# Optimization experiments

Hardware: AMD Instinct MI355X
Metric: run time of the kernel (lower is better)

Reference implementation:

```python
import jax, jax.numpy as jnp
import numpy as np
import math

BATCH, TBINS, SPATIAL = 16, 8, 16
WIN, SHIFT = 8, 4
DIM, HEADS = 1024, 16
HD = DIM // HEADS
N = WIN * WIN          # tokens per window = 64
NW = (SPATIAL // WIN) ** 2  # windows per image = 4
HIDDEN = 4 * DIM


def _static_buffers():
    ws = WIN
    # continuous relative coords table (signed log-spaced), [(2ws-1)^2, 2]
    c = np.arange(-(ws - 1), ws, dtype=np.float32) / (ws - 1)
    c = np.sign(c) * np.log2(1.0 + np.abs(c))
    gh, gw = np.meshgrid(c, c, indexing='ij')
    table = np.stack([gh, gw], axis=-1).reshape(-1, 2).astype(np.float32)
    # relative position index, [N, N]
    coords = np.stack(np.meshgrid(np.arange(ws), np.arange(ws), indexing='ij')).reshape(2, -1)
    rel = (coords[:, :, None] - coords[:, None, :]).transpose(1, 2, 0)
    rel[..., 0] += ws - 1
    rel[..., 1] += ws - 1
    rel[..., 0] *= 2 * ws - 1
    rp_idx = rel.sum(-1)  # [N, N] int
    # shifted-window attention mask, [NW, N, N]
    img = np.zeros((SPATIAL, SPATIAL), dtype=np.float32)
    slices = [slice(0, -ws), slice(-ws, -SHIFT), slice(-SHIFT, None)]
    cnt = 0
    for hs in slices:
        for wsl in slices:
            img[hs, wsl] = cnt
            cnt += 1
    mw = img.reshape(SPATIAL // ws, ws, SPATIAL // ws, ws).transpose(0, 2, 1, 3).reshape(-1, ws * ws)
    diff = mw[:, None, :] - mw[:, :, None]  # matches unsqueeze(1) - unsqueeze(2)
    attn_mask = np.where(diff != 0, np.float32(-100.0), np.float32(0.0))
    return jnp.asarray(table), jnp.asarray(rp_idx), jnp.asarray(attn_mask)

CPB_TABLE, RP_IDX, ATTN_MASK = _static_buffers()


def _window_partition(x):  # [B, H, W, C] -> [B*nW, ws, ws, C]
    b, h, w, c = x.shape
    x = x.reshape(b, h // WIN, WIN, w // WIN, WIN, c).transpose(0, 1, 3, 2, 4, 5)
    return x.reshape(-1, WIN, WIN, c)


def _window_reverse(win, h, w):  # [B*nW, ws, ws, C] -> [B, H, W, C]
    b = win.shape[0] // ((h // WIN) * (w // WIN))
    x = win.reshape(b, h // WIN, w // WIN, WIN, WIN, -1).transpose(0, 1, 3, 2, 4, 5)
    return x.reshape(b, h, w, -1)


def _layernorm(x, g, b):
    m = jnp.mean(x, -1, keepdims=True)
    v = jnp.mean((x - m) ** 2, -1, keepdims=True)
    return (x - m) * jax.lax.rsqrt(v + 1e-5) * g + b


def _l2norm(x):
    return x / jnp.maximum(jnp.linalg.norm(x, axis=-1, keepdims=True), 1e-12)


def setup_inputs() -> dict:
    key = jax.random.key(0)
    ks = jax.random.split(key, 16)
    s = 0.02
    inp = {
        'x': jax.random.normal(ks[0], (BATCH, TBINS * SPATIAL * SPATIAL, DIM), jnp.float32),
        'qkv_w': jax.random.normal(ks[1], (3 * DIM, DIM), jnp.float32) * s,
        'q_bias': jnp.zeros((DIM,), jnp.float32),
        'v_bias': jnp.zeros((DIM,), jnp.float32),
        'logit_scale': jnp.full((HEADS, 1, 1), math.log(10.0), jnp.float32),
        'cpb_w1': jax.random.normal(ks[2], (512, 2), jnp.float32) * s,
        'cpb_b1': jnp.zeros((512,), jnp.float32),
        'cpb_w2': jax.random.normal(ks[3], (HEADS, 512), jnp.float32) * s,
        'proj_w': jax.random.normal(ks[4], (DIM, DIM), jnp.float32) * s,
        'proj_b': jnp.zeros((DIM,), jnp.float32),
        'norm1_w': jnp.ones((DIM,), jnp.float32),
        'norm1_b': jnp.zeros((DIM,), jnp.float32),
        'fc1_w': jax.random.normal(ks[5], (HIDDEN, DIM), jnp.float32) * s,
        'fc1_b': jnp.zeros((HIDDEN,), jnp.float32),
        'fc2_w': jax.random.normal(ks[6], (DIM, HIDDEN), jnp.float32) * s,
        'fc2_b': jnp.zeros((DIM,), jnp.float32),
        'norm2_w': jnp.ones((DIM,), jnp.float32),
        'norm2_b': jnp.zeros((DIM,), jnp.float32),
    }
    return inp


def reference(x, qkv_w, q_bias, v_bias, logit_scale, cpb_w1, cpb_b1, cpb_w2,
              proj_w, proj_b, norm1_w, norm1_b, fc1_w, fc1_b, fc2_w, fc2_b,
              norm2_w, norm2_b):
    B, L, C = x.shape
    xs = x.reshape(B * TBINS, SPATIAL, SPATIAL, C)
    shortcut = xs
    # cyclic shift
    shifted = jnp.roll(xs, shift=(-SHIFT, -SHIFT), axis=(1, 2))
    xw = _window_partition(shifted).reshape(-1, N, C)  # [Bw, N, C]
    Bw = xw.shape[0]

    # qkv with q/v bias only (no k bias)
    qkv_bias = jnp.concatenate([q_bias, jnp.zeros_like(v_bias), v_bias])
    qkv = xw @ qkv_w.T + qkv_bias
    qkv = qkv.reshape(Bw, N, 3, HEADS, HD).transpose(2, 0, 3, 1, 4)
    q, k, v = qkv[0], qkv[1], qkv[2]  # [Bw, h, N, hd]

    # cosine attention with clamped learnable logit scale
    attn = jnp.einsum('bhnd,bhmd->bhnm', _l2norm(q), _l2norm(k))
    scale = jnp.exp(jnp.minimum(logit_scale, math.log(100.0)))  # [h,1,1]
    attn = attn * scale[None]

    # continuous relative position bias via CPB-MLP
    tbl = jax.nn.relu(CPB_TABLE @ cpb_w1.T + cpb_b1) @ cpb_w2.T  # [(2ws-1)^2, h]
    tbl = 16.0 * jax.nn.sigmoid(tbl)
    bias = tbl[RP_IDX.reshape(-1)].reshape(N, N, HEADS).transpose(2, 0, 1)  # [h,N,N]
    attn = attn + bias[None]

    # shift mask
    attn = attn.reshape(Bw // NW, NW, HEADS, N, N) + ATTN_MASK[None, :, None]
    attn = attn.reshape(Bw, HEADS, N, N)
    attn = jax.nn.softmax(attn, axis=-1)

    out = jnp.einsum('bhnm,bhmd->bhnd', attn, v)
    out = out.transpose(0, 2, 1, 3).reshape(Bw, N, C)
    out = out @ proj_w.T + proj_b

    out = _window_reverse(out.reshape(-1, WIN, WIN, C), SPATIAL, SPATIAL)
    out = jnp.roll(out, shift=(SHIFT, SHIFT), axis=(1, 2))

    # SwinV2 post-norm residuals
    xs = shortcut + _layernorm(out, norm1_w, norm1_b)
    h = jax.nn.gelu(xs @ fc1_w.T + fc1_b, approximate=False) @ fc2_w.T + fc2_b
    xs = xs + _layernorm(h, norm2_w, norm2_b)
    return xs.reshape(B, L, C)
```

## Files before the change

### kernel.cpp

```cpp
#include <hip/hip_runtime.h>
#include <hip/hip_bf16.h>
#include <math.h>

typedef __hip_bfloat16 bf16;
typedef __attribute__((ext_vector_type(8))) short short8;
typedef __attribute__((ext_vector_type(4))) short short4v;
typedef __attribute__((ext_vector_type(4))) float floatx4;
typedef __attribute__((ext_vector_type(2))) unsigned int uint2v;

#define DEV static __device__ __forceinline__

DEV float bf2f(unsigned short u) {
  union { unsigned int i; float f; } x;
  x.i = ((unsigned int)u) << 16;
  return x.f;
}
DEV unsigned short f2bf_bits(float f) {
  union { bf16 h; unsigned short u; } x;
  x.h = __float2bfloat16(f);
  return x.u;
}
DEV short8 cvt8(float4 a, float4 b) {
  short8 r;
  r[0] = (short)f2bf_bits(a.x); r[1] = (short)f2bf_bits(a.y);
  r[2] = (short)f2bf_bits(a.z); r[3] = (short)f2bf_bits(a.w);
  r[4] = (short)f2bf_bits(b.x); r[5] = (short)f2bf_bits(b.y);
  r[6] = (short)f2bf_bits(b.z); r[7] = (short)f2bf_bits(b.w);
  return r;
}

DEV float gelu_fast(float v) {
  float y = v * (1.5957691216f + 0.0713548163f * v * v);
  return __fdividef(v, 1.f + __expf(-y));
}

DEV void gload_lds16(const unsigned short* g, unsigned short* l) {
  __builtin_amdgcn_global_load_lds((const __attribute__((address_space(1))) void*)g,
                                   (__attribute__((address_space(3))) void*)l,
                                   16, 0, 0);
}

DEV unsigned lds_addr(const void* p) {
  return (unsigned)(unsigned long long)(const __attribute__((address_space(3))) char*)p;
}

DEV int gather_win_row(int wr) {
  int bw = wr >> 6, n = wr & 63;
  int bt = bw >> 2, w2 = bw & 3;
  int wi = w2 >> 1, wj = w2 & 1;
  int r = n >> 3, c = n & 7;
  int sr = (wi * 8 + r + 4) & 15;
  int sc = (wj * 8 + c + 4) & 15;
  return bt * 256 + sr * 16 + sc;
}

enum { BIAS_SIMPLE = 0, BIAS_QKV = 1 };
enum { ACT_NONE = 0, ACT_GELU = 1 };

__global__ __launch_bounds__(256) void cvt_bf16(const float* __restrict__ in,
                                                bf16* __restrict__ out, int n) {
  int i = (blockIdx.x * 256 + threadIdx.x) * 8;
  if (i >= n) return;
  float4 a = *reinterpret_cast<const float4*>(in + i);
  float4 b = *reinterpret_cast<const float4*>(in + i + 4);
  *reinterpret_cast<short8*>((unsigned short*)out + i) = cvt8(a, b);
}

#define VMCNT(N_) asm volatile("s_waitcnt vmcnt(" #N_ ")" ::: "memory")
#define WAITLGKM() do { asm volatile("s_waitcnt lgkmcnt(0)" ::: "memory"); \
                        __builtin_amdgcn_sched_barrier(0); } while (0)
#define BARRIER() __builtin_amdgcn_s_barrier()
#define DSR(dst, addr, OFF) \
  asm volatile("ds_read_b128 %0, %1 offset:" #OFF : "=v"(dst) : "v"(addr) : "memory")

#define STG8(BUF, ISB, KS, KT) do { \
    unsigned short* d_ = (unsigned short*)(smem + (BUF) * 65536 + (ISB) * 32768 + (KS) * 16384); \
    gload_lds16(((ISB) ? bgp[0] : agp[0]) + (KT) * 64 + (KS) * 32, d_ + tid * 8); \
    gload_lds16(((ISB) ? bgp[1] : agp[1]) + (KT) * 64 + (KS) * 32, d_ + 4096 + tid * 8); \
  } while (0)

#define RD_A8(CUR, KS, IH) do { \
    unsigned a_ = smemBase + (CUR) * 65536 + (KS) * 16384 + aB0 + (IH) * 4096; \
    DSR(af[0], a_, 0); DSR(af[1], a_, 1024); DSR(af[2], a_, 2048); DSR(af[3], a_, 3072); \
  } while (0)

#define RD_B8(CUR, KS) do { \
    unsigned b_ = smemBase + (CUR) * 65536 + 32768 + (KS) * 16384 + bB0; \
    DSR(bfr[0], b_, 0); DSR(bfr[1], b_, 1024); DSR(bfr[2], b_, 2048); DSR(bfr[3], b_, 3072); \
  } while (0)

#define MFMA16(IH) do { \
    __builtin_amdgcn_s_setprio(1); \
    _Pragma("unroll") \
    for (int i_ = 0; i_ < 4; ++i_) \
      _Pragma("unroll") \
      for (int j_ = 0; j_ < 4; ++j_) \
        acc[(IH) * 4 + i_][j_] = __builtin_amdgcn_mfma_f32_16x16x32_bf16( \
            af[i_], bfr[j_], acc[(IH) * 4 + i_][j_], 0, 0, 0); \
    __builtin_amdgcn_s_setprio(0); \
  } while (0)

template <int GATHER, int BIASMODE, int ACT>
__global__ __launch_bounds__(512, 2) void gemm8p(
    const unsigned short* __restrict__ A, const unsigned short* __restrict__ B,
    const float* __restrict__ bias0, const float* __restrict__ bias1,
    bf16* __restrict__ C, int M, int N, int K)
{
  extern __shared__ __align__(16) char smem[];
  const int tid = threadIdx.x;
  const int lane = tid & 63;
  const int wave = tid >> 6;
  const int wm = wave >> 2, wn = wave & 3;
  const int l15 = lane & 15, g = lane >> 4;
  const int xr = (l15 >> 1) & 3;

  const int gy = gridDim.y;
  const int nwg = gridDim.x * gy;
  int lin = blockIdx.y * gridDim.x + blockIdx.x;
  if ((nwg & 7) == 0) lin = (lin & 7) * (nwg >> 3) + (lin >> 3);
  const int tileM = (lin / gy) * 256;
  const int tileN = (lin % gy) * 256;

  const unsigned short* agp[2];
  const unsigned short* bgp[2];
#pragma unroll
  for (int u = 0; u < 2; ++u) {
    int s = u * 512 + tid;
    int row = s >> 2;
    int dslot = (s & 3) ^ ((s >> 3) & 3);
    int gr = tileM + row;
    int sr = GATHER ? gather_win_row(gr) : gr;
    agp[u] = A + (size_t)sr * (size_t)K + dslot * 8;
    bgp[u] = B + (size_t)(tileN + row) * (size_t)K + dslot * 8;
  }

  const unsigned smemBase = lds_addr(smem);
  const unsigned aB0 = (unsigned)((wm * 128 + l15) * 64 + ((g ^ xr) * 16));
  const unsigned bB0 = (unsigned)((wn * 64 + l15) * 64 + ((g ^ xr) * 16));

  floatx4 acc[8][4];
#pragma unroll
  for (int i = 0; i < 8; ++i)
#pragma unroll
    for (int j = 0; j < 4; ++j) acc[i][j] = (floatx4){0.f, 0.f, 0.f, 0.f};

  short8 af[4], bfr[4];
  const int NT = K >> 6;
  int cur = 0;

  STG8(0, 0, 0, 0); STG8(0, 1, 0, 0); STG8(0, 0, 1, 0); STG8(0, 1, 1, 0);
  VMCNT(0);
  BARRIER();

  for (int t = 0; t < NT - 1; ++t) {
    const int nb = cur ^ 1;
    RD_B8(cur, 0); RD_A8(cur, 0, 0);
    STG8(nb, 0, 0, t + 1);
    BARRIER(); WAITLGKM(); MFMA16(0); BARRIER();
    RD_A8(cur, 0, 1);
    STG8(nb, 1, 0, t + 1);
    VMCNT(4);
    BARRIER(); WAITLGKM(); MFMA16(1); BARRIER();
    RD_B8(cur, 1); RD_A8(cur, 1, 0);
    STG8(nb, 0, 1, t + 1);
    BARRIER(); WAITLGKM(); MFMA16(0); BARRIER();
    RD_A8(cur, 1, 1);
    STG8(nb, 1, 1, t + 1);
    VMCNT(4);
    BARRIER(); WAITLGKM(); MFMA16(1); BARRIER();
    cur = nb;
  }
  RD_B8(cur, 0); RD_A8(cur, 0, 0);
  BARRIER(); WAITLGKM(); MFMA16(0); BARRIER();
  RD_A8(cur, 0, 1);
  VMCNT(0);
  BARRIER(); WAITLGKM(); MFMA16(1); BARRIER();
  RD_B8(cur, 1); RD_A8(cur, 1, 0);
  BARRIER(); WAITLGKM(); MFMA16(0); BARRIER();
  RD_A8(cur, 1, 1);
  WAITLGKM(); MFMA16(1);

  __syncthreads();
  unsigned short* sh16 = (unsigned short*)smem;
  const int q = l15;
  float bv[4];
#pragma unroll
  for (int j = 0; j < 4; ++j) {
    const int colG = tileN + wn * 64 + j * 16 + q;
    if (BIASMODE == BIAS_QKV) {
      bv[j] = (colG < 1024) ? bias0[colG] : (colG < 2048 ? 0.f : bias1[colG - 2048]);
    } else {
      bv[j] = bias0[colG];
    }
  }
#pragma unroll
  for (int h = 0; h < 2; ++h) {
    if (wm == h) {
#pragma unroll
      for (int i = 0; i < 8; ++i)
#pragma unroll
        for (int j = 0; j < 4; ++j)
#pragma unroll
          for (int r = 0; r < 4; ++r) {
            float v = acc[i][j][r] + bv[j];
            if (ACT == ACT_GELU) v = gelu_fast(v);
            sh16[(i * 16 + g * 4 + r) * 264 + wn * 64 + j * 16 + q] = f2bf_bits(v);
          }
    }
    __syncthreads();
#pragma unroll
    for (int pass = 0; pass < 8; ++pass) {
      const int idx = pass * 512 + tid;
      const int row = idx >> 5, c16 = idx & 31;
      uint4 val = *reinterpret_cast<const uint4*>(&sh16[row * 264 + c16 * 8]);
      *reinterpret_cast<uint4*>(
          (unsigned short*)C + (size_t)(tileM + h * 128 + row) * (size_t)N +
          tileN + c16 * 8) = val;
    }
    __syncthreads();
  }
}

template <int GATHER, int BIASMODE, int ACT>
__global__ __launch_bounds__(256, 2) void gemm_bt(
    const unsigned short* __restrict__ A, const unsigned short* __restrict__ B,
    const float* __restrict__ bias0, const float* __restrict__ bias1,
    bf16* __restrict__ C, int M, int N, int K)
{
  __shared__ __align__(16) unsigned short sh[128 * 136];
  unsigned short* As = sh;
  unsigned short* Bs = sh + 8192;

  const int tid = threadIdx.x;
  const int lane = tid & 63;
  const int wave = tid >> 6;
  const int waveM = wave >> 1, waveN = wave & 1;
  const int tileM = blockIdx.x * 128, tileN = blockIdx.y * 128;

  const int row0 = tid >> 3;
  const int kOff = (tid & 7) * 8;

  const unsigned short* ag[4];
  const unsigned short* bg[4];
  unsigned short* al[4];
  unsigned short* bl[4];
#pragma unroll
  for (int t = 0; t < 4; ++t) {
    int gr = tileM + row0 + 32 * t;
    int sr = GATHER ? gather_win_row(gr) : gr;
    ag[t] = A + (size_t)sr * (size_t)K + (size_t)kOff;
    bg[t] = B + (size_t)(tileN + row0 + 32 * t) * (size_t)K + (size_t)kOff;
    al[t] = &As[(row0 + 32 * t) * 64 + kOff];
    bl[t] = &Bs[(row0 + 32 * t) * 64 + kOff];
  }

  floatx4 acc[4][4];
#pragma unroll
  for (int i = 0; i < 4; ++i)
#pragma unroll
    for (int j = 0; j < 4; ++j) acc[i][j] = (floatx4){0.f, 0.f, 0.f, 0.f};

  for (int k0 = 0; k0 < K; k0 += 64) {
#pragma unroll
    for (int t = 0; t < 4; ++t) {
      gload_lds16(ag[t] + k0, al[t]);
      gload_lds16(bg[t] + k0, bl[t]);
    }
    __syncthreads();
#pragma unroll
    for (int ks = 0; ks < 2; ++ks) {
      const int kk = ks * 32 + (lane >> 4) * 8;
      short8 afv[4], bfv[4];
#pragma unroll
      for (int i = 0; i < 4; ++i)
        afv[i] = *reinterpret_cast<const short8*>(
            &As[(waveM * 64 + i * 16 + (lane & 15)) * 64 + kk]);
#pragma unroll
      for (int j = 0; j < 4; ++j)
        bfv[j] = *reinterpret_cast<const short8*>(
            &Bs[(waveN * 64 + j * 16 + (lane & 15)) * 64 + kk]);
#pragma unroll
      for (int i = 0; i < 4; ++i)
#pragma unroll
        for (int j = 0; j < 4; ++j)
          acc[i][j] = __builtin_amdgcn_mfma_f32_16x16x32_bf16(afv[i], bfv[j], acc[i][j], 0, 0, 0);
    }
    __syncthreads();
  }

#pragma unroll
  for (int j = 0; j < 4; ++j) {
    const int colL = waveN * 64 + j * 16 + (lane & 15);
    const int colG = tileN + colL;
    float bv;
    if (BIASMODE == BIAS_QKV) {
      if (colG < 1024) bv = bias0[colG];
      else if (colG < 2048) bv = 0.f;
      else bv = bias1[colG - 2048];
    } else {
      bv = bias0[colG];
    }
#pragma unroll
    for (int i = 0; i < 4; ++i) {
      const int rL = waveM * 64 + i * 16 + ((lane >> 4) * 4);
#pragma unroll
      for (int r = 0; r < 4; ++r) {
        float v = acc[i][j][r] + bv;
        if (ACT == ACT_GELU) v = gelu_fast(v);
        sh[(rL + r) * 136 + colL] = f2bf_bits(v);
      }
    }
  }
  __syncthreads();
  {
    const int rowR = tid >> 4;
    const int colR = (tid & 15) * 8;
#pragma unroll
    for (int s = 0; s < 8; ++s) {
      const int row = s * 16 + rowR;
      uint4 val = *reinterpret_cast<const uint4*>(&sh[row * 136 + colR]);
      *reinterpret_cast<uint4*>(
          (unsigned short*)C + (size_t)(tileM + row) * (size_t)N + tileN + colR) = val;
    }
  }
}

__global__ __launch_bounds__(512) void cpb_kernel(
    const float* __restrict__ w1, const float* __restrict__ b1,
    const float* __restrict__ w2, float* __restrict__ TBL)
{
  __shared__ float hid[512];
  const int i = blockIdx.x;
  const int j = threadIdx.x;
  const float d0 = ((float)(i / 15) - 7.f) / 7.f;
  const float d1 = ((float)(i % 15) - 7.f) / 7.f;
  const float t0 = copysignf(log2f(1.f + fabsf(d0)), d0);
  const float t1 = copysignf(log2f(1.f + fabsf(d1)), d1);
  float hv = t0 * w1[j * 2] + t1 * w1[j * 2 + 1] + b1[j];
  hid[j] = fmaxf(hv, 0.f);
  __syncthreads();
  if (j < 16) {
    float s = 0.f;
    for (int jj = 0; jj < 512; ++jj) s += w2[j * 512 + jj] * hid[jj];
    TBL[j * 225 + i] = 16.f / (1.f + expf(-s));
  }
}

__global__ __launch_bounds__(256) void attn_mfma(
    const bf16* __restrict__ QKV, const float* __restrict__ TBL,
    const float* __restrict__ ls, bf16* __restrict__ ATT)
{
  __shared__ __align__(16) unsigned short Ps[4][64][72];
  __shared__ float tbs[4][226];
  __shared__ int ids[64];

  const int tid = threadIdx.x;
  const int w = tid >> 6;
  const int l = tid & 63;
  const int q = l & 15;
  const int g = l >> 4;
  const int bw = blockIdx.x >> 2;
  const int h = (blockIdx.x & 3) * 4 + w;

  const unsigned short* qkvu = (const unsigned short*)QKV;
  const size_t rbase = (size_t)(bw * 64) * 3072;

  if (tid < 64) {
    const int w2 = bw & 3, wi = w2 >> 1, wj = w2 & 1;
    const int r = tid >> 3, c = tid & 7;
    const int rr = (wi == 0) ? 0 : (r < 4 ? 1 : 2);
    const int rc = (wj == 0) ? 0 : (c < 4 ? 1 : 2);
    ids[tid] = rr * 3 + rc;
  }
#pragma unroll
  for (int i = 0; i < 4; ++i) {
    int idx = i * 64 + l;
    if (idx < 225) tbs[w][idx] = TBL[h * 225 + idx];
  }
  __syncthreads();

  short8 kf[4][2], qf[4][2];
#pragma unroll
  for (int i = 0; i < 4; ++i) {
    const unsigned short* rp = qkvu + rbase + (size_t)(16 * i + q) * 3072 + h * 64 + g * 8;
    qf[i][0] = *reinterpret_cast<const short8*>(rp);
    qf[i][1] = *reinterpret_cast<const short8*>(rp + 32);
    kf[i][0] = *reinterpret_cast<const short8*>(rp + 1024);
    kf[i][1] = *reinterpret_cast<const short8*>(rp + 1024 + 32);
  }

  float rk4[4], rq4[4];
#pragma unroll
  for (int i = 0; i < 4; ++i) {
    float sk = 0.f, sq = 0.f;
#pragma unroll
    for (int ks = 0; ks < 2; ++ks)
#pragma unroll
      for (int e = 0; e < 8; ++e) {
        float kv = bf2f((unsigned short)kf[i][ks][e]);
        float qv = bf2f((unsigned short)qf[i][ks][e]);
        sk += kv * kv; sq += qv * qv;
      }
    sk += __shfl_xor(sk, 16); sk += __shfl_xor(sk, 32);
    sq += __shfl_xor(sq, 16); sq += __shfl_xor(sq, 32);
    rk4[i] = 1.f / fmaxf(sqrtf(sk), 1e-12f);
    rq4[i] = 1.f / fmaxf(sqrtf(sq), 1e-12f);
  }
  const float scl = expf(fminf(ls[h], 4.60517019f));
  float rqs[4];
#pragma unroll
  for (int j = 0; j < 4; ++j) rqs[j] = rq4[j] * scl;

  floatx4 acc[4][4];
#pragma unroll
  for (int i = 0; i < 4; ++i)
#pragma unroll
    for (int j = 0; j < 4; ++j) acc[i][j] = (floatx4){0.f, 0.f, 0.f, 0.f};
#pragma unroll
  for (int ks = 0; ks < 2; ++ks)
#pragma unroll
    for (int i = 0; i < 4; ++i)
#pragma unroll
      for (int j = 0; j < 4; ++j)
        acc[i][j] = __builtin_amdgcn_mfma_f32_16x16x32_bf16(kf[i][ks], qf[j][ks], acc[i][j], 0, 0, 0);

  short8 vf[4][2];
  const unsigned short* vbase = qkvu + rbase + 2048 + h * 64;
#pragma unroll
  for (int jp = 0; jp < 4; ++jp)
#pragma unroll
    for (int ks = 0; ks < 2; ++ks) {
      const int m0 = ks * 32 + g * 8;
      const unsigned short* vp = vbase + 16 * jp + q;
      union { short8 v; unsigned short u[8]; } pk;
#pragma unroll
      for (int e = 0; e < 8; ++e)
        pk.u[e] = vp[(size_t)(m0 + e) * 3072];
      vf[jp][ks] = pk.v;
    }

  int idn[4], rtn[4], ctn[4];
#pragma unroll
  for (int j = 0; j < 4; ++j) {
    const int n = 16 * j + q;
    rtn[j] = n >> 3; ctn[j] = n & 7; idn[j] = ids[n];
  }
#pragma unroll
  for (int i = 0; i < 4; ++i) {
#pragma unroll
    for (int r = 0; r < 4; ++r) {
      const int m = 16 * i + 4 * g + r;
      const float rkm = __shfl(rk4[i], 4 * g + r);
      const int rm = m >> 3, cm = m & 7;
      const int idm = ids[m];
#pragma unroll
      for (int j = 0; j < 4; ++j) {
        float v = acc[i][j][r] * (rkm * rqs[j]) +
                  tbs[w][(rtn[j] - rm + 7) * 15 + (ctn[j] - cm + 7)];
        if (idm != idn[j]) v -= 100.f;
        acc[i][j][r] = v;
      }
    }
  }

  float rs4[4];
#pragma unroll
  for (int j = 0; j < 4; ++j) {
    float mx = acc[0][j][0];
#pragma unroll
    for (int i = 0; i < 4; ++i)
#pragma unroll
      for (int r = 0; r < 4; ++r) mx = fmaxf(mx, acc[i][j][r]);
    mx = fmaxf(mx, __shfl_xor(mx, 16));
    mx = fmaxf(mx, __shfl_xor(mx, 32));
    float sm = 0.f;
#pragma unroll
    for (int i = 0; i < 4; ++i)
#pragma unroll
      for (int r = 0; r < 4; ++r) {
        float e = __expf(acc[i][j][r] - mx);
        acc[i][j][r] = e; sm += e;
      }
    sm += __shfl_xor(sm, 16);
    sm += __shfl_xor(sm, 32);
    rs4[j] = 1.f / sm;
  }

#pragma unroll
  for (int j = 0; j < 4; ++j)
#pragma unroll
    for (int i = 0; i < 4; ++i) {
      uint2v pw;
      pw[0] = (unsigned int)f2bf_bits(acc[i][j][0]) |
              ((unsigned int)f2bf_bits(acc[i][j][1]) << 16);
      pw[1] = (unsigned int)f2bf_bits(acc[i][j][2]) |
              ((unsigned int)f2bf_bits(acc[i][j][3]) << 16);
      *reinterpret_cast<uint2v*>(&Ps[w][16 * j + q][16 * i + 4 * g]) = pw;
    }

  floatx4 o[4][4];
#pragma unroll
  for (int i = 0; i < 4; ++i)
#pragma unroll
    for (int j = 0; j < 4; ++j) o[i][j] = (floatx4){0.f, 0.f, 0.f, 0.f};
#pragma unroll
  for (int ks = 0; ks < 2; ++ks) {
    short8 pa[4];
#pragma unroll
    for (int i2 = 0; i2 < 4; ++i2)
      pa[i2] = *reinterpret_cast<const short8*>(&Ps[w][16 * i2 + q][ks * 32 + g * 8]);
#pragma unroll
    for (int i2 = 0; i2 < 4; ++i2)
#pragma unroll
      for (int j2 = 0; j2 < 4; ++j2)
        o[i2][j2] = __builtin_amdgcn_mfma_f32_16x16x32_bf16(pa[i2], vf[j2][ks], o[i2][j2], 0, 0, 0);
  }

  unsigned short* op = (unsigned short*)ATT + (size_t)(bw * 64) * 1024 + h * 64;
#pragma unroll
  for (int i2 = 0; i2 < 4; ++i2)
#pragma unroll
    for (int r = 0; r < 4; ++r) {
      const float rsn = __shfl(rs4[i2], 4 * g + r);
      const int row = 16 * i2 + 4 * g + r;
#pragma unroll
      for (int j2 = 0; j2 < 4; ++j2)
        op[(size_t)row * 1024 + 16 * j2 + q] = f2bf_bits(o[i2][j2][r] * rsn);
    }
}

template <bool GATHER, bool WB>
__global__ __launch_bounds__(256) void ln_residual(
    const bf16* __restrict__ src, const float* base,
    const float* __restrict__ gw, const float* __restrict__ gb,
    float* out, bf16* __restrict__ out_bf)
{
  const int tok = blockIdx.x * 4 + (threadIdx.x >> 6);
  const int lane = threadIdx.x & 63;
  int srow;
  if (GATHER) {
    const int bt = tok >> 8, rem = tok & 255, i = rem >> 4, j = rem & 15;
    const int p = (i + 12) & 15, qq = (j + 12) & 15;
    srow = (bt * 4 + (p >> 3) * 2 + (qq >> 3)) * 64 + (p & 7) * 8 + (qq & 7);
  } else {
    srow = tok;
  }
  const unsigned short* sp = (const unsigned short*)src + (size_t)srow * 1024 + lane * 16;
  short8 lv0 = *reinterpret_cast<const short8*>(sp);
  short8 lv1 = *reinterpret_cast<const short8*>(sp + 8);
  float v[16];
  float s = 0.f, sq = 0.f;
#pragma unroll
  for (int u = 0; u < 8; ++u) {
    float f = bf2f((unsigned short)lv0[u]); v[u] = f; s += f; sq += f * f;
    float g = bf2f((unsigned short)lv1[u]); v[u + 8] = g; s += g; sq += g * g;
  }
#pragma unroll
  for (int off = 32; off > 0; off >>= 1) { s += __shfl_xor(s, off); sq += __shfl_xor(sq, off); }
  const float mean = s * (1.f / 1024.f);
  const float var = sq * (1.f / 1024.f) - mean * mean;
  const float rstd = rsqrtf(var + 1e-5f);

  const float* bp = base + (size_t)tok * 1024 + lane * 16;
  float* op = out + (size_t)tok * 1024 + lane * 16;
  unsigned short* obp = WB ? ((unsigned short*)out_bf + (size_t)tok * 1024 + lane * 16) : nullptr;
  union { short8 v; unsigned short u[8]; } ob0, ob1;
#pragma unroll
  for (int q4 = 0; q4 < 4; ++q4) {
    float4 b4 = *reinterpret_cast<const float4*>(bp + q4 * 4);
    float bl[4] = {b4.x, b4.y, b4.z, b4.w};
    float4 o4;
    float* ol = (float*)&o4;
#pragma unroll
    for (int u = 0; u < 4; ++u) {
      const int c = lane * 16 + q4 * 4 + u;
      ol[u] = bl[u] + (v[q4 * 4 + u] - mean) * rstd * gw[c] + gb[c];
      if (WB) {
        if (q4 < 2) ob0.u[q4 * 4 + u] = f2bf_bits(ol[u]);
        else ob1.u[(q4 - 2) * 4 + u] = f2bf_bits(ol[u]);
      }
    }
    *reinterpret_cast<float4*>(op + q4 * 4) = o4;
  }
  if (WB) {
    *reinterpret_cast<short8*>(obp) = ob0.v;
    *reinterpret_cast<short8*>(obp + 8) = ob1.v;
  }
}

extern "C" void kernel_launch(void* const* d_in, const int* in_sizes, int n_in,
                              void* d_out, int out_size, void* d_ws, size_t ws_size,
                              hipStream_t stream) {
  (void)in_sizes; (void)n_in; (void)out_size;
  const float* x      = (const float*)d_in[0];
  const float* qkv_w  = (const float*)d_in[1];
  const float* q_bias = (const float*)d_in[2];
  const float* v_bias = (const float*)d_in[3];
  const float* lscale = (const float*)d_in[4];
  const float* cpb_w1 = (const float*)d_in[5];
  const float* cpb_b1 = (const float*)d_in[6];
  const float* cpb_w2 = (const float*)d_in[7];
  const float* proj_w = (const float*)d_in[8];
  const float* proj_b = (const float*)d_in[9];
  const float* n1w    = (const float*)d_in[10];
  const float* n1b    = (const float*)d_in[11];
  const float* fc1_w  = (const float*)d_in[12];
  const float* fc1_b  = (const float*)d_in[13];
  const float* fc2_w  = (const float*)d_in[14];
  const float* fc2_b  = (const float*)d_in[15];
  const float* n2w    = (const float*)d_in[16];
  const float* n2b    = (const float*)d_in[17];
  float* out = (float*)d_out;

  static int attr_ok = -1;
  if (attr_ok < 0) {
    hipError_t e1 = hipFuncSetAttribute(
        reinterpret_cast<const void*>(&gemm8p<1, BIAS_QKV, ACT_NONE>),
        hipFuncAttributeMaxDynamicSharedMemorySize, 131072);
    hipError_t e2 = hipFuncSetAttribute(
        reinterpret_cast<const void*>(&gemm8p<0, BIAS_SIMPLE, ACT_NONE>),
        hipFuncAttributeMaxDynamicSharedMemorySize, 131072);
    hipError_t e3 = hipFuncSetAttribute(
        reinterpret_cast<const void*>(&gemm8p<0, BIAS_SIMPLE, ACT_GELU>),
        hipFuncAttributeMaxDynamicSharedMemorySize, 131072);
    attr_ok = (e1 == hipSuccess && e2 == hipSuccess && e3 == hipSuccess) ? 1 : 0;
  }

  char* ws = (char*)d_ws;
  bf16*  QKV  = (bf16*)(ws);
  bf16*  H    = (bf16*)(ws);
  bf16*  ATT  = (bf16*)(ws + 67108864);
  bf16*  XSB  = (bf16*)(ws + 67108864);
  bf16*  F2   = (bf16*)(ws + 67108864);
  bf16*  XBF  = (bf16*)(ws + 83886080);
  bf16*  PROJ = (bf16*)(ws + 83886080);
  float* TBL  = (float*)(ws + 100663296);

  const bool persist = ws_size >= (size_t)125845504;
  bf16* WQKV, *WPROJ, *WF1, *WF2;
  if (persist) {
    WQKV  = (bf16*)(ws + 100679680);
    WPROJ = (bf16*)(ws + 106971136);
    WF1   = (bf16*)(ws + 109068288);
    WF2   = (bf16*)(ws + 117456896);
  } else {
    WQKV  = (bf16*)(ws + 67108864);
    WPROJ = (bf16*)(ws + 50331648);
    WF1   = (bf16*)(ws + 83886080);
    WF2   = (bf16*)(ws + 83886080 + 8388608);
  }

  cpb_kernel<<<225, 512, 0, stream>>>(cpb_w1, cpb_b1, cpb_w2, TBL);
  if (persist) {
    cvt_bf16<<<1536, 256, 0, stream>>>(qkv_w, WQKV, 3145728);
    cvt_bf16<<<512, 256, 0, stream>>>(proj_w, WPROJ, 1048576);
    cvt_bf16<<<2048, 256, 0, stream>>>(fc1_w, WF1, 4194304);
    cvt_bf16<<<2048, 256, 0, stream>>>(fc2_w, WF2, 4194304);
  }

  for (int ch = 0; ch < 4; ++ch) {
    const size_t tokBase = (size_t)ch * 8192;
    const float* x_c = x + tokBase * 1024;
    float* out_c = out + tokBase * 1024;

    cvt_bf16<<<4096, 256, 0, stream>>>(x_c, XBF, 8388608);
    if (!persist) {
      cvt_bf16<<<1536, 256, 0, stream>>>(qkv_w, WQKV, 3145728);
      cvt_bf16<<<512, 256, 0, stream>>>(proj_w, WPROJ, 1048576);
    }

    if (attr_ok) {
      gemm8p<1, BIAS_QKV, ACT_NONE><<<dim3(32, 12), 512, 131072, stream>>>(
          (const unsigned short*)XBF, (const unsigned short*)WQKV,
          q_bias, v_bias, QKV, 8192, 3072, 1024);
    } else {
      gemm_bt<1, BIAS_QKV, ACT_NONE><<<dim3(64, 24), 256, 0, stream>>>(
          (const unsigned short*)XBF, (const unsigned short*)WQKV,
          q_bias, v_bias, QKV, 8192, 3072, 1024);
    }
    attn_mfma<<<512, 256, 0, stream>>>(QKV, TBL, lscale, ATT);
    if (attr_ok) {
      gemm8p<0, BIAS_SIMPLE, ACT_NONE><<<dim3(32, 4), 512, 131072, stream>>>(
          (const unsigned short*)ATT, (const unsigned short*)WPROJ,
          proj_b, nullptr, PROJ, 8192, 1024, 1024);
    } else {
      gemm_bt<0, BIAS_SIMPLE, ACT_NONE><<<dim3(64, 8), 256, 0, stream>>>(
          (const unsigned short*)ATT, (const unsigned short*)WPROJ,
          proj_b, nullptr, PROJ, 8192, 1024, 1024);
    }
    ln_residual<true, true><<<2048, 256, 0, stream>>>(PROJ, x_c, n1w, n1b, out_c, XSB);
    if (!persist) {
      cvt_bf16<<<2048, 256, 0, stream>>>(fc1_w, WF1, 4194304);
      cvt_bf16<<<2048, 256, 0, stream>>>(fc2_w, WF2, 4194304);
    }
    if (attr_ok) {
      gemm8p<0, BIAS_SIMPLE, ACT_GELU><<<dim3(32, 16), 512, 131072, stream>>>(
          (const unsigned short*)XSB, (const unsigned short*)WF1,
          fc1_b, nullptr, H, 8192, 4096, 1024);
      gemm8p<0, BIAS_SIMPLE, ACT_NONE><<<dim3(32, 4), 512, 131072, stream>>>(
          (const unsigned short*)H, (const unsigned short*)WF2,
          fc2_b, nullptr, F2, 8192, 1024, 4096);
    } else {
      gemm_bt<0, BIAS_SIMPLE, ACT_GELU><<<dim3(64, 32), 256, 0, stream>>>(
          (const unsigned short*)XSB, (const unsigned short*)WF1,
          fc1_b, nullptr, H, 8192, 4096, 1024);
      gemm_bt<0, BIAS_SIMPLE, ACT_NONE><<<dim3(64, 8), 256, 0, stream>>>(
          (const unsigned short*)H, (const unsigned short*)WF2,
          fc2_b, nullptr, F2, 8192, 1024, 4096);
    }
    ln_residual<false, false><<<2048, 256, 0, stream>>>(F2, out_c, n2w, n2b, out_c, nullptr);
  }
}
```

Measured before the change: 1.713 ms.

## Add narrower 256x128 GEMM tile variant for QKV, proj and fc2

```diff
diff --git a/kernel.cpp b/kernel.cpp
--- a/kernel.cpp
+++ b/kernel.cpp
@@ -213,6 +213,159 @@
       const int idx = pass * 512 + tid;
       const int row = idx >> 5, c16 = idx & 31;
       uint4 val = *reinterpret_cast<const uint4*>(&sh16[row * 264 + c16 * 8]);
+      *reinterpret_cast<uint4*>(
+          (unsigned short*)C + (size_t)(tileM + h * 128 + row) * (size_t)N +
+          tileN + c16 * 8) = val;
+    }
+    __syncthreads();
+  }
+}
+
+#define STG_A2(BUF, KS, KT) do { \
+    unsigned short* d_ = (unsigned short*)(smem + (BUF) * 49152 + (KS) * 16384); \
+    gload_lds16(agp[0] + (KT) * 64 + (KS) * 32, d_ + tid * 8); \
+    gload_lds16(agp[1] + (KT) * 64 + (KS) * 32, d_ + 4096 + tid * 8); \
+  } while (0)
+
+#define STG_B1(BUF, KS, KT) do { \
+    unsigned short* d_ = (unsigned short*)(smem + (BUF) * 49152 + 32768 + (KS) * 8192); \
+    gload_lds16(bgp0 + (KT) * 64 + (KS) * 32, d_ + tid * 8); \
+  } while (0)
+
+#define RD_A8N(CUR, KS, IH) do { \
+    unsigned a_ = smemBase + (CUR) * 49152 + (KS) * 16384 + aB0 + (IH) * 4096; \
+    DSR(af[0], a_, 0); DSR(af[1], a_, 1024); DSR(af[2], a_, 2048); DSR(af[3], a_, 3072); \
+  } while (0)
+
+#define RD_B2N(CUR, KS) do { \
+    unsigned b_ = smemBase + (CUR) * 49152 + 32768 + (KS) * 8192 + bB0; \
+    DSR(bfr[0], b_, 0); DSR(bfr[1], b_, 1024); \
+  } while (0)
+
+#define MFMA8(IH) do { \
+    __builtin_amdgcn_s_setprio(1); \
+    _Pragma("unroll") \
+    for (int i_ = 0; i_ < 4; ++i_) \
+      _Pragma("unroll") \
+      for (int j_ = 0; j_ < 2; ++j_) \
+        acc[(IH) * 4 + i_][j_] = __builtin_amdgcn_mfma_f32_16x16x32_bf16( \
+            af[i_], bfr[j_], acc[(IH) * 4 + i_][j_], 0, 0, 0); \
+    __builtin_amdgcn_s_setprio(0); \
+  } while (0)
+
+template <int GATHER, int BIASMODE, int ACT>
+__global__ __launch_bounds__(512, 2) void gemm8pn(
+    const unsigned short* __restrict__ A, const unsigned short* __restrict__ B,
+    const float* __restrict__ bias0, const float* __restrict__ bias1,
+    bf16* __restrict__ C, int M, int N, int K)
+{
+  extern __shared__ __align__(16) char smem[];
+  const int tid = threadIdx.x;
+  const int lane = tid & 63;
+  const int wave = tid >> 6;
+  const int wm = wave >> 2, wn = wave & 3;
+  const int l15 = lane & 15, g = lane >> 4;
+  const int xr = (l15 >> 1) & 3;
+
+  const int gy = gridDim.y;
+  const int nwg = gridDim.x * gy;
+  int lin = blockIdx.y * gridDim.x + blockIdx.x;
+  if ((nwg & 7) == 0) lin = (lin & 7) * (nwg >> 3) + (lin >> 3);
+  const int tileM = (lin / gy) * 256;
+  const int tileN = (lin % gy) * 128;
+
+  const unsigned short* agp[2];
+#pragma unroll
+  for (int u = 0; u < 2; ++u) {
+    int s = u * 512 + tid;
+    int row = s >> 2;
+    int dslot = (s & 3) ^ ((s >> 3) & 3);
+    int gr = tileM + row;
+    int sr = GATHER ? gather_win_row(gr) : gr;
+    agp[u] = A + (size_t)sr * (size_t)K + dslot * 8;
+  }
+  const unsigned short* bgp0 =
+      B + (size_t)(tileN + (tid >> 2)) * (size_t)K + ((tid & 3) ^ ((tid >> 3) & 3)) * 8;
+
+  const unsigned smemBase = lds_addr(smem);
+  const unsigned aB0 = (unsigned)((wm * 128 + l15) * 64 + ((g ^ xr) * 16));
+  const unsigned bB0 = (unsigned)((wn * 32 + l15) * 64 + ((g ^ xr) * 16));
+
+  floatx4 acc[8][2];
+#pragma unroll
+  for (int i = 0; i < 8; ++i)
+#pragma unroll
+    for (int j = 0; j < 2; ++j) acc[i][j] = (floatx4){0.f, 0.f, 0.f, 0.f};
+
+  short8 af[4], bfr[2];
+  const int NT = K >> 6;
+  int cur = 0;
+
+  STG_A2(0, 0, 0); STG_B1(0, 0, 0); STG_A2(0, 1, 0); STG_B1(0, 1, 0);
+  VMCNT(0);
+  BARRIER();
+
+  for (int t = 0; t < NT - 1; ++t) {
+    const int nb = cur ^ 1;
+    RD_B2N(cur, 0); RD_A8N(cur, 0, 0);
+    STG_A2(nb, 0, t + 1);
+    BARRIER(); WAITLGKM(); MFMA8(0); BARRIER();
+    RD_A8N(cur, 0, 1);
+    STG_B1(nb, 0, t + 1);
+    VMCNT(3);
+    BARRIER(); WAITLGKM(); MFMA8(1); BARRIER();
+    RD_B2N(cur, 1); RD_A8N(cur, 1, 0);
+    STG_A2(nb, 1, t + 1);
+    BARRIER(); WAITLGKM(); MFMA8(0); BARRIER();
+    RD_A8N(cur, 1, 1);
+    STG_B1(nb, 1, t + 1);
+    VMCNT(3);
+    BARRIER(); WAITLGKM(); MFMA8(1); BARRIER();
+    cur = nb;
+  }
+  RD_B2N(cur, 0); RD_A8N(cur, 0, 0);
+  BARRIER(); WAITLGKM(); MFMA8(0); BARRIER();
+  RD_A8N(cur, 0, 1);
+  VMCNT(0);
+  BARRIER(); WAITLGKM(); MFMA8(1); BARRIER();
+  RD_B2N(cur, 1); RD_A8N(cur, 1, 0);
+  BARRIER(); WAITLGKM(); MFMA8(0); BARRIER();
+  RD_A8N(cur, 1, 1);
+  WAITLGKM(); MFMA8(1);
+
+  __syncthreads();
+  unsigned short* sh16 = (unsigned short*)smem;
+  const int q = l15;
+  float bv[2];
+#pragma unroll
+  for (int j = 0; j < 2; ++j) {
+    const int colG = tileN + wn * 32 + j * 16 + q;
+    if (BIASMODE == BIAS_QKV) {
+      bv[j] = (colG < 1024) ? bias0[colG] : (colG < 2048 ? 0.f : bias1[colG - 2048]);
+    } else {
+      bv[j] = bias0[colG];
+    }
+  }
+#pragma unroll
+  for (int h = 0; h < 2; ++h) {
+    if (wm == h) {
+#pragma unroll
+      for (int i = 0; i < 8; ++i)
+#pragma unroll
+        for (int j = 0; j < 2; ++j)
+#pragma unroll
+          for (int r = 0; r < 4; ++r) {
+            float v = acc[i][j][r] + bv[j];
+            if (ACT == ACT_GELU) v = gelu_fast(v);
+            sh16[(i * 16 + g * 4 + r) * 136 + wn * 32 + j * 16 + q] = f2bf_bits(v);
+          }
+    }
+    __syncthreads();
+#pragma unroll
+    for (int pass = 0; pass < 4; ++pass) {
+      const int idx = pass * 512 + tid;
+      const int row = idx >> 4, c16 = idx & 15;
+      uint4 val = *reinterpret_cast<const uint4*>(&sh16[row * 136 + c16 * 8]);
       *reinterpret_cast<uint4*>(
           (unsigned short*)C + (size_t)(tileM + h * 128 + row) * (size_t)N +
           tileN + c16 * 8) = val;
@@ -615,14 +768,14 @@
   static int attr_ok = -1;
   if (attr_ok < 0) {
     hipError_t e1 = hipFuncSetAttribute(
-        reinterpret_cast<const void*>(&gemm8p<1, BIAS_QKV, ACT_NONE>),
+        reinterpret_cast<const void*>(&gemm8p<0, BIAS_SIMPLE, ACT_GELU>),
         hipFuncAttributeMaxDynamicSharedMemorySize, 131072);
     hipError_t e2 = hipFuncSetAttribute(
-        reinterpret_cast<const void*>(&gemm8p<0, BIAS_SIMPLE, ACT_NONE>),
-        hipFuncAttributeMaxDynamicSharedMemorySize, 131072);
+        reinterpret_cast<const void*>(&gemm8pn<1, BIAS_QKV, ACT_NONE>),
+        hipFuncAttributeMaxDynamicSharedMemorySize, 98304);
     hipError_t e3 = hipFuncSetAttribute(
-        reinterpret_cast<const void*>(&gemm8p<0, BIAS_SIMPLE, ACT_GELU>),
-        hipFuncAttributeMaxDynamicSharedMemorySize, 131072);
+        reinterpret_cast<const void*>(&gemm8pn<0, BIAS_SIMPLE, ACT_NONE>),
+        hipFuncAttributeMaxDynamicSharedMemorySize, 98304);
     attr_ok = (e1 == hipSuccess && e2 == hipSuccess && e3 == hipSuccess) ? 1 : 0;
   }
 
@@ -670,7 +823,7 @@
     }
 
     if (attr_ok) {
-      gemm8p<1, BIAS_QKV, ACT_NONE><<<dim3(32, 12), 512, 131072, stream>>>(
+      gemm8pn<1, BIAS_QKV, ACT_NONE><<<dim3(32, 24), 512, 98304, stream>>>(
           (const unsigned short*)XBF, (const unsigned short*)WQKV,
           q_bias, v_bias, QKV, 8192, 3072, 1024);
     } else {
@@ -680,7 +833,7 @@
     }
     attn_mfma<<<512, 256, 0, stream>>>(QKV, TBL, lscale, ATT);
     if (attr_ok) {
-      gemm8p<0, BIAS_SIMPLE, ACT_NONE><<<dim3(32, 4), 512, 131072, stream>>>(
+      gemm8pn<0, BIAS_SIMPLE, ACT_NONE><<<dim3(32, 8), 512, 98304, stream>>>(
           (const unsigned short*)ATT, (const unsigned short*)WPROJ,
           proj_b, nullptr, PROJ, 8192, 1024, 1024);
     } else {
@@ -697,7 +850,7 @@
       gemm8p<0, BIAS_SIMPLE, ACT_GELU><<<dim3(32, 16), 512, 131072, stream>>>(
           (const unsigned short*)XSB, (const unsigned short*)WF1,
           fc1_b, nullptr, H, 8192, 4096, 1024);
-      gemm8p<0, BIAS_SIMPLE, ACT_NONE><<<dim3(32, 4), 512, 131072, stream>>>(
+      gemm8pn<0, BIAS_SIMPLE, ACT_NONE><<<dim3(32, 8), 512, 98304, stream>>>(
           (const unsigned short*)H, (const unsigned short*)WF2,
           fc2_b, nullptr, F2, 8192, 1024, 4096);
     } else {
```

New measurement: 1.575 ms. -8.0%, faster.
